# Optimization experiments

Measured on AMD Instinct MI355X. Metric: run time of the kernel, lower is better.

Reference implementation:

```python
import jax, jax.numpy as jnp
import numpy as np
from math import sqrt

RELATIVE_CUTOFF = 128
VALUE_DIM = 64


def _skew(m):
    # m: (b, h, S, 2S-1) -> (b, h, S, S), out[i, j] = m[i, j - i + S - 1]
    b, h, S, _ = m.shape
    m = jnp.pad(m, ((0, 0), (0, 0), (0, 0), (0, 1)))          # (b,h,S,2S)
    m = m.reshape(b, h, 2 * S * S)
    m = jnp.pad(m, ((0, 0), (0, 0), (0, S - 1)))
    m = m.reshape(b, h, S + 1, 2 * S - 1)
    return m[:, :, :S, S - 1:]


def setup_inputs() -> dict:
    key = jax.random.key(0)
    ks = jax.random.split(key, 5)
    B, S, E, H, Dk, Dv = 2, 2048, 512, 8, 64, 64
    return {
        "xs": jax.random.normal(ks[0], (B, S, E), dtype=jnp.float32),
        "w_q": jax.random.normal(ks[1], (H, E, Dk), dtype=jnp.float32) * (1.0 / sqrt(E)),
        "w_k": jax.random.normal(ks[2], (H, E, Dk), dtype=jnp.float32) * (1.0 / sqrt(E)),
        "w_v": jax.random.normal(ks[3], (H, E, Dv), dtype=jnp.float32) * (1.0 / sqrt(E)),
        "w_o": jnp.ones((H,), dtype=jnp.float32),
        "a_k": jax.random.normal(ks[4], (2 * RELATIVE_CUTOFF + 1, Dk), dtype=jnp.float32) * 0.1,
    }


def reference(xs, w_q, w_k, w_v, w_o, a_k):
    S = xs.shape[1]
    queries = jnp.einsum("bse,heq->bhsq", xs, w_q)
    keys = jnp.einsum("bse,hek->bhsk", xs, w_k)
    values = jnp.einsum("bse,hev->bhsv", xs, w_v)

    # relative positional embeddings: pos in [-S+1, S-1], clamped to cutoff
    pos = jnp.clip(jnp.arange(-S + 1, S), -RELATIVE_CUTOFF, RELATIVE_CUTOFF) + RELATIVE_CUTOFF
    rel = a_k[pos]                                             # (2S-1, Dk)

    q_k = jnp.einsum("bhiq,bhjq->bhij", queries, keys)
    q_rel = _skew(jnp.einsum("bhiq,rq->bhir", queries, rel))   # (b,h,S,S)

    e = (q_k + q_rel) / sqrt(VALUE_DIM)
    alphas = jax.nn.softmax(e, axis=3)
    z = jnp.einsum("bhij,bhjv->bhiv", alphas, values)
    return jnp.einsum("bhsv,h->bsv", z, w_o)
```

## Files before the change

kernel.cpp:

```cpp
#include <hip/hip_runtime.h>
#include <hip/hip_bf16.h>

#define S_LEN 2048
#define E_DIM 512
#define D_DIM 64
#define H_NUM 8
#define B_NUM 2
#define BH_NUM 16
#define NQA 257
#define QAE_W 512
#define KSPLIT 2
#define NT (S_LEN / KSPLIT / 64)
#define QTILE 256

typedef _Float16 half8 __attribute__((ext_vector_type(8)));
typedef float f32x16 __attribute__((ext_vector_type(16)));
typedef unsigned int uint2v __attribute__((ext_vector_type(2)));
typedef unsigned int uint4v __attribute__((ext_vector_type(4)));

static __device__ __forceinline__ f32x16 MFMA(half8 a, half8 b, f32x16 c) {
    return __builtin_amdgcn_mfma_f32_32x32x16_f16(a, b, c, 0, 0, 0);
}
static __device__ __forceinline__ f32x16 ZERO16() {
    f32x16 z;
    #pragma unroll
    for (int i = 0; i < 16; ++i) z[i] = 0.f;
    return z;
}
static __device__ __forceinline__ unsigned int PKRTZ(float a, float b) {
    return __builtin_bit_cast(unsigned int, __builtin_amdgcn_cvt_pkrtz(a, b));
}

__global__ __launch_bounds__(256) void cast_x_kernel(
    const float* __restrict__ xs, _Float16* __restrict__ Xh)
{
    const int idx = (blockIdx.x * 256 + threadIdx.x) * 8;
    float4 a = *(const float4*)&xs[idx];
    float4 b = *(const float4*)&xs[idx + 4];
    half8 o;
    o[0] = (_Float16)a.x; o[1] = (_Float16)a.y; o[2] = (_Float16)a.z; o[3] = (_Float16)a.w;
    o[4] = (_Float16)b.x; o[5] = (_Float16)b.y; o[6] = (_Float16)b.z; o[7] = (_Float16)b.w;
    *(half8*)&Xh[idx] = o;
}

__global__ __launch_bounds__(256) void cast_wak_kernel(
    const float* __restrict__ w_q, const float* __restrict__ w_k,
    const float* __restrict__ w_v, const float* __restrict__ w_o,
    const float* __restrict__ a_k,
    _Float16* __restrict__ Wht, _Float16* __restrict__ akh)
{
    __shared__ float T[64][68];
    const int type = blockIdx.z;
    const int t = threadIdx.x;
    if (type == 3) {
        const int bn = blockIdx.y * 8 + blockIdx.x;
        if (bn >= 9) return;
        const int idx = (bn * 256 + t) * 8;
        if (idx < NQA * 64) {
            float4 a = *(const float4*)&a_k[idx];
            float4 b = *(const float4*)&a_k[idx + 4];
            half8 o;
            o[0] = (_Float16)a.x; o[1] = (_Float16)a.y; o[2] = (_Float16)a.z; o[3] = (_Float16)a.w;
            o[4] = (_Float16)b.x; o[5] = (_Float16)b.y; o[6] = (_Float16)b.z; o[7] = (_Float16)b.w;
            *(half8*)&akh[idx] = o;
        }
        return;
    }
    const int kt = blockIdx.x, h = blockIdx.y;
    const float* W = (type == 0) ? w_q : (type == 1) ? w_k : w_v;
    const float scale = (type == 0) ? 0.125f : (type == 2 ? w_o[h] : 1.0f);
    const int kr = t >> 2, nseg = (t & 3) * 16;
    #pragma unroll
    for (int i = 0; i < 4; ++i)
        *(float4*)&T[kr][nseg + 4 * i] =
            *(const float4*)&W[((size_t)h * 512 + kt * 64 + kr) * 64 + nseg + 4 * i];
    __syncthreads();
    const int nr = t >> 2, kseg = (t & 3) * 16;
    _Float16* dst = Wht + ((size_t)(type * 8 + h) * 64 + nr) * 512 + kt * 64 + kseg;
    #pragma unroll
    for (int i = 0; i < 2; ++i) {
        half8 o;
        #pragma unroll
        for (int j = 0; j < 8; ++j) o[j] = (_Float16)(T[kseg + 8 * i + j][nr] * scale);
        *(half8*)&dst[8 * i] = o;
    }
}

__global__ __launch_bounds__(256) void proj_mfma_kernel(
    const _Float16* __restrict__ Xh, const _Float16* __restrict__ Wht,
    const _Float16* __restrict__ akh,
    _Float16* __restrict__ Qh, _Float16* __restrict__ Kh,
    _Float16* __restrict__ Vt, _Float16* __restrict__ QAe)
{
    __shared__ __align__(16) _Float16 raw[30208];
    _Float16 (*Xlds)[128][72] = (_Float16(*)[128][72])raw;
    _Float16 (*Wlds)[64][72]  = (_Float16(*)[64][72])(raw + 18432);
    _Float16* ob  = raw;
    _Float16 (*ak)[72] = (_Float16(*)[72])(raw + 9216);
    _Float16* SLo = raw + 29952;
    _Float16* SHi = raw + 30080;

    const int mt = blockIdx.x, bh = blockIdx.y, type = blockIdx.z;
    const int b = bh >> 3, h = bh & 7;
    const int m0 = mt * 128;
    const int t = threadIdx.x, wid = t >> 6, lane = t & 63;
    const int lq = lane & 31, lh = lane >> 5;

    const _Float16* W = Wht + (size_t)(type * 8 + h) * 64 * 512;
    const _Float16* X = Xh + ((size_t)b * S_LEN + m0) * 512;

    const int xrow = t >> 1, xseg = (t & 1) * 32;
    const int wrow = t >> 2, wseg = (t & 3) * 16;

    #pragma unroll
    for (int i = 0; i < 4; ++i)
        *(half8*)&Xlds[0][xrow][xseg + 8 * i] =
            *(const half8*)&X[(size_t)xrow * 512 + xseg + 8 * i];
    #pragma unroll
    for (int i = 0; i < 2; ++i)
        *(half8*)&Wlds[0][wrow][wseg + 8 * i] =
            *(const half8*)&W[(size_t)wrow * 512 + wseg + 8 * i];
    __syncthreads();

    f32x16 acc[2];
    acc[0] = ZERO16(); acc[1] = ZERO16();
    int cur = 0;
    for (int c = 0; c < 8; ++c) {
        half8 xst[4], wst[2];
        if (c < 7) {
            const int k0 = (c + 1) * 64;
            #pragma unroll
            for (int i = 0; i < 4; ++i)
                xst[i] = *(const half8*)&X[(size_t)xrow * 512 + k0 + xseg + 8 * i];
            #pragma unroll
            for (int i = 0; i < 2; ++i)
                wst[i] = *(const half8*)&W[(size_t)wrow * 512 + k0 + wseg + 8 * i];
        }
        #pragma unroll
        for (int kc = 0; kc < 4; ++kc) {
            half8 a  = *(const half8*)&Xlds[cur][wid * 32 + lq][kc * 16 + lh * 8];
            half8 b0 = *(const half8*)&Wlds[cur][lq][kc * 16 + lh * 8];
            half8 b1 = *(const half8*)&Wlds[cur][32 + lq][kc * 16 + lh * 8];
            acc[0] = MFMA(a, b0, acc[0]);
            acc[1] = MFMA(a, b1, acc[1]);
        }
        if (c < 7) {
            #pragma unroll
            for (int i = 0; i < 4; ++i)
                *(half8*)&Xlds[cur ^ 1][xrow][xseg + 8 * i] = xst[i];
            #pragma unroll
            for (int i = 0; i < 2; ++i)
                *(half8*)&Wlds[cur ^ 1][wrow][wseg + 8 * i] = wst[i];
        }
        __syncthreads();
        cur ^= 1;
    }

    #pragma unroll
    for (int n = 0; n < 2; ++n)
        #pragma unroll
        for (int r = 0; r < 16; ++r) {
            int row = wid * 32 + (r & 3) + ((r >> 2) << 3) + (lh << 2);
            ob[row * 72 + n * 32 + lq] = (_Float16)acc[n][r];
        }
    __syncthreads();

    if (type == 2) {
        const int v = t >> 2, sseg = (t & 3) * 32;
        _Float16* dst = Vt + ((size_t)bh * 64 + v) * S_LEN + m0 + sseg;
        #pragma unroll
        for (int i = 0; i < 4; ++i) {
            half8 o;
            #pragma unroll
            for (int j = 0; j < 8; ++j) o[j] = ob[(sseg + 8 * i + j) * 72 + v];
            *(half8*)&dst[8 * i] = o;
        }
        return;
    }

    {
        _Float16* P = (type == 0) ? Qh : Kh;
        const int row = t >> 1, seg = (t & 1) * 32;
        _Float16* dst = P + ((size_t)bh * S_LEN + m0 + row) * 64 + seg;
        #pragma unroll
        for (int i = 0; i < 4; ++i)
            *(half8*)&dst[8 * i] = *(const half8*)&ob[row * 72 + seg + 8 * i];
    }
    if (type != 0) return;

    for (int r = t; r < 288; r += 256) {
        if (r < NQA) {
            #pragma unroll
            for (int i = 0; i < 8; ++i)
                *(half8*)&ak[r][8 * i] = *(const half8*)&akh[(size_t)r * 64 + 8 * i];
        } else {
            half8 z = {};
            #pragma unroll
            for (int i = 0; i < 8; ++i) *(half8*)&ak[r][8 * i] = z;
        }
    }
    __syncthreads();

    half8 qfr[4];
    #pragma unroll
    for (int kc = 0; kc < 4; ++kc)
        qfr[kc] = *(const half8*)&ob[(wid * 32 + lq) * 72 + kc * 16 + lh * 8];

    for (int nsub = 0; nsub < 9; ++nsub) {
        f32x16 qa = ZERO16();
        #pragma unroll
        for (int kc = 0; kc < 4; ++kc) {
            half8 bf = *(const half8*)&ak[nsub * 32 + lq][kc * 16 + lh * 8];
            qa = MFMA(qfr[kc], bf, qa);
        }
        const int col = nsub * 32 + lq;
        if (col < NQA) {
            #pragma unroll
            for (int r = 0; r < 16; ++r) {
                const int row = m0 + wid * 32 + (r & 3) + ((r >> 2) << 3) + (lh << 2);
                const _Float16 v = (_Float16)qa[r];
                QAe[((size_t)bh * S_LEN + row) * QAE_W + col + 128] = v;
                if (col == 0)   SLo[row - m0] = v;
                if (col == 256) SHi[row - m0] = v;
            }
        }
    }
    __syncthreads();

    const int prow = t >> 1, pseg = (t & 1) * 64;
    const _Float16 lo = SLo[prow], hi = SHi[prow];
    half8 vlo, vhi;
    #pragma unroll
    for (int j = 0; j < 8; ++j) { vlo[j] = lo; vhi[j] = hi; }
    _Float16* pb = QAe + ((size_t)bh * S_LEN + m0 + prow) * QAE_W;
    #pragma unroll
    for (int i = 0; i < 8; ++i) {
        *(half8*)&pb[pseg + 8 * i] = vlo;
        *(half8*)&pb[384 + pseg + 8 * i] = vhi;
    }
}

__global__ __launch_bounds__(512) void attn_kernel(
    const _Float16* __restrict__ Qh, const _Float16* __restrict__ Kh,
    const _Float16* __restrict__ Vt, const _Float16* __restrict__ QAe,
    _Float16* __restrict__ Po, float2* __restrict__ Ml)
{
    __shared__ __align__(16) char smraw[36864];
    _Float16 (*Klds)[64][72] = (_Float16(*)[64][72])smraw;
    _Float16 (*Vlds)[64][72] = (_Float16(*)[64][72])(smraw + 18432);
    _Float16* Obuf = (_Float16*)smraw;
    __shared__ __align__(16) _Float16 Bnd[8][32][128];

    const int p0 = blockIdx.x;
    const int nb = (p0 & 7) * 32 + (p0 >> 3);
    const int bh = nb >> 4;
    const int rem = nb & 15;
    const int qt = rem & 7, ks = rem >> 3;
    const int i0 = qt * QTILE;

    const int t = threadIdx.x, wid = t >> 6, lane = t & 63;
    const int lq = lane & 31, lh = lane >> 5;
    const int i0w = i0 + wid * 32;
    const int qg = i0w + lq;

    half8 qf[4];
    #pragma unroll
    for (int kc = 0; kc < 4; ++kc)
        qf[kc] = *(const half8*)&Qh[((size_t)bh * S_LEN + qg) * 64 + kc * 16 + lh * 8];

    const _Float16* qaeRow = QAe + ((size_t)bh * S_LEN + qg) * QAE_W;
    const float qa_lo = (float)qaeRow[128];
    const float qa_hi = (float)qaeRow[384];
    const _Float16* BndSrc = QAe + ((size_t)bh * S_LEN + i0w) * QAE_W;

    float rm = -1e30f, rl = 0.f;
    f32x16 acco[2];
    acco[0] = ZERO16(); acco[1] = ZERO16();

    const int srow = t >> 3, sseg = (t & 7) * 8;
    const _Float16* Kbase = Kh + (size_t)bh * S_LEN * 64;
    const _Float16* Vbase = Vt + ((size_t)bh * 64 + srow) * S_LEN;

    const int brow = lane >> 4;
    const int bcol = (lane & 15) * 8;

    half8 kst, vst, breg[8];
    const int kv0 = ks * 64;
    *(half8*)&Klds[0][srow][sseg] = *(const half8*)&Kbase[(size_t)(kv0 + srow) * 64 + sseg];
    *(half8*)&Vlds[0][srow][sseg] = *(const half8*)&Vbase[kv0 + sseg];
    kst = *(const half8*)&Kbase[(size_t)(kv0 + 128 + srow) * 64 + sseg];
    vst = *(const half8*)&Vbase[kv0 + 128 + sseg];

    bool inb_next;
    {
        const int d0 = kv0 - i0w;
        inb_next = (d0 < 159) && (d0 > -191);
        if (inb_next) {
            const int cw0n = (d0 + 225) & ~7;
            #pragma unroll
            for (int ps = 0; ps < 8; ++ps)
                breg[ps] = *(const half8*)&BndSrc[(size_t)(ps * 4 + brow) * QAE_W + cw0n + bcol];
        }
    }
    __syncthreads();

    for (int jt = 0; jt < NT; ++jt) {
        const int cur = jt & 1;
        if (jt) __syncthreads();
        if (jt + 1 < NT) {
            *(half8*)&Klds[cur ^ 1][srow][sseg] = kst;
            *(half8*)&Vlds[cur ^ 1][srow][sseg] = vst;
        }
        if (jt + 2 < NT) {
            const int jg = kv0 + (jt + 2) * 128;
            kst = *(const half8*)&Kbase[(size_t)(jg + srow) * 64 + sseg];
            vst = *(const half8*)&Vbase[jg + sseg];
        }

        const int diff = kv0 + jt * 128 - i0w;
        const bool inband = inb_next;
        const int cw0 = (diff + 225) & ~7;

        if (inband) {
            #pragma unroll
            for (int ps = 0; ps < 8; ++ps)
                *(half8*)&Bnd[wid][ps * 4 + brow][bcol] = breg[ps];
        }
        {
            const int dn = diff + 128;
            inb_next = (jt + 1 < NT) && (dn < 159) && (dn > -191);
            if (inb_next) {
                const int cw0n = (dn + 225) & ~7;
                #pragma unroll
                for (int ps = 0; ps < 8; ++ps)
                    breg[ps] = *(const half8*)&BndSrc[(size_t)(ps * 4 + brow) * QAE_W + cw0n + bcol];
            }
        }

        f32x16 accs[2];
        accs[0] = ZERO16(); accs[1] = ZERO16();
        __builtin_amdgcn_s_setprio(1);
        #pragma unroll
        for (int kc = 0; kc < 4; ++kc) {
            half8 ka = *(const half8*)&Klds[cur][lq][kc * 16 + lh * 8];
            half8 kb = *(const half8*)&Klds[cur][32 + lq][kc * 16 + lh * 8];
            accs[0] = MFMA(ka, qf[kc], accs[0]);
            accs[1] = MFMA(kb, qf[kc], accs[1]);
        }
        __builtin_amdgcn_s_setprio(0);

        const bool allhi = (diff >= 159);
        const bool alllo = (diff <= -191);
        float bunif = 0.f;
        if (allhi) bunif = qa_hi;
        else if (alllo) bunif = qa_lo;
        else {
            asm volatile("s_waitcnt lgkmcnt(0)" ::: "memory");
            __builtin_amdgcn_sched_barrier(0);
            const int pb = diff + 256 - cw0 - lq;
            #pragma unroll
            for (int m = 0; m < 2; ++m)
                #pragma unroll
                for (int r = 0; r < 16; ++r) {
                    const int keyoff = m * 32 + (r & 3) + ((r >> 2) << 3) + (lh << 2);
                    accs[m][r] += (float)Bnd[wid][lq][pb + keyoff];
                }
        }

        float t8[8];
        #pragma unroll
        for (int i = 0; i < 8; ++i)
            t8[i] = fmaxf(fmaxf(accs[0][i], accs[0][i + 8]),
                          fmaxf(accs[1][i], accs[1][i + 8]));
        float tmax = fmaxf(fmaxf(fmaxf(t8[0], t8[1]), fmaxf(t8[2], t8[3])),
                           fmaxf(fmaxf(t8[4], t8[5]), fmaxf(t8[6], t8[7])));
        tmax = fmaxf(tmax, __shfl_xor(tmax, 32));
        const float mnew = fmaxf(rm, tmax + bunif);
        const bool resc = __any(mnew > rm);
        const float corr = __expf(rm - mnew);
        const float shift = mnew - bunif;
        rm = mnew;

        #pragma unroll
        for (int m = 0; m < 2; ++m)
            #pragma unroll
            for (int r = 0; r < 16; ++r)
                accs[m][r] = __expf(accs[m][r] - shift);

        float s8[8];
        #pragma unroll
        for (int i = 0; i < 8; ++i)
            s8[i] = (accs[0][i] + accs[0][i + 8]) + (accs[1][i] + accs[1][i + 8]);
        float psum = ((s8[0] + s8[1]) + (s8[2] + s8[3])) +
                     ((s8[4] + s8[5]) + (s8[6] + s8[7]));
        psum += __shfl_xor(psum, 32);

        if (resc) {
            rl = rl * corr + psum;
            #pragma unroll
            for (int n = 0; n < 2; ++n)
                #pragma unroll
                for (int r = 0; r < 16; ++r) acco[n][r] *= corr;
        } else {
            rl += psum;
        }

        half8 pf[4];
        #pragma unroll
        for (int kc = 0; kc < 4; ++kc) {
            const int m = kc >> 1, rb = (kc & 1) * 8;
            unsigned int a01 = PKRTZ(accs[m][rb + 0], accs[m][rb + 1]);
            unsigned int a45 = PKRTZ(accs[m][rb + 4], accs[m][rb + 5]);
            unsigned int a23 = PKRTZ(accs[m][rb + 2], accs[m][rb + 3]);
            unsigned int a67 = PKRTZ(accs[m][rb + 6], accs[m][rb + 7]);
            uint2v r02 = __builtin_amdgcn_permlane32_swap(a01, a45, false, false);
            uint2v r13 = __builtin_amdgcn_permlane32_swap(a23, a67, false, false);
            uint4v wv;
            wv[0] = r02[0]; wv[1] = r13[0]; wv[2] = r02[1]; wv[3] = r13[1];
            pf[kc] = __builtin_bit_cast(half8, wv);
        }

        __builtin_amdgcn_s_setprio(1);
        #pragma unroll
        for (int kc = 0; kc < 4; ++kc) {
            half8 v0 = *(const half8*)&Vlds[cur][lq][kc * 16 + lh * 8];
            half8 v1 = *(const half8*)&Vlds[cur][32 + lq][kc * 16 + lh * 8];
            acco[0] = MFMA(v0, pf[kc], acco[0]);
            acco[1] = MFMA(v1, pf[kc], acco[1]);
        }
        __builtin_amdgcn_s_setprio(0);
    }

    __syncthreads();
    const int orow = wid * 32 + lq;
    #pragma unroll
    for (int n = 0; n < 2; ++n)
        #pragma unroll
        for (int rq = 0; rq < 4; ++rq) {
            uint2v hv;
            hv[0] = PKRTZ(acco[n][rq * 4 + 0], acco[n][rq * 4 + 1]);
            hv[1] = PKRTZ(acco[n][rq * 4 + 2], acco[n][rq * 4 + 3]);
            *(uint2v*)&Obuf[(size_t)orow * 72 + n * 32 + rq * 8 + lh * 4] = hv;
        }
    if (lh == 0)
        Ml[((size_t)ks * BH_NUM + bh) * S_LEN + qg] = make_float2(rm, rl);
    asm volatile("s_waitcnt lgkmcnt(0)" ::: "memory");
    __builtin_amdgcn_sched_barrier(0);
    const int rrow = wid * 32 + (lane >> 1);
    const int rseg = (lane & 1) * 32;
    _Float16* dst = Po + (((size_t)ks * BH_NUM + bh) * S_LEN + i0 + rrow) * 64 + rseg;
    #pragma unroll
    for (int i = 0; i < 4; ++i)
        *(half8*)&dst[8 * i] = *(const half8*)&Obuf[(size_t)rrow * 72 + rseg + 8 * i];
}

__global__ __launch_bounds__(256) void merge_kernel(
    const _Float16* __restrict__ Po, const float2* __restrict__ Ml,
    float* __restrict__ out)
{
    const int b = blockIdx.y;
    const int s = blockIdx.x * 32 + (threadIdx.x >> 3);
    const int v0 = (threadIdx.x & 7) * 8;
    float acc[8] = {0, 0, 0, 0, 0, 0, 0, 0};
    #pragma unroll
    for (int h = 0; h < 8; ++h) {
        const int bh = b * 8 + h;
        float m[KSPLIT], l[KSPLIT];
        #pragma unroll
        for (int p = 0; p < KSPLIT; ++p) {
            const float2 v = Ml[((size_t)p * BH_NUM + bh) * S_LEN + s];
            m[p] = v.x; l[p] = v.y;
        }
        float M = fmaxf(m[0], m[1]);
        float L = 0.f, w[KSPLIT];
        #pragma unroll
        for (int p = 0; p < KSPLIT; ++p) { w[p] = __expf(m[p] - M); L += w[p] * l[p]; }
        const float invL = 1.0f / L;
        #pragma unroll
        for (int p = 0; p < KSPLIT; ++p) {
            half8 o = *(const half8*)&Po[(((size_t)p * BH_NUM + bh) * S_LEN + s) * 64 + v0];
            const float wp = w[p] * invL;
            #pragma unroll
            for (int j = 0; j < 8; ++j) acc[j] += wp * (float)o[j];
        }
    }
    float4 o0 = {acc[0], acc[1], acc[2], acc[3]};
    float4 o1 = {acc[4], acc[5], acc[6], acc[7]};
    *(float4*)&out[((size_t)b * S_LEN + s) * 64 + v0] = o0;
    *(float4*)&out[((size_t)b * S_LEN + s) * 64 + v0 + 4] = o1;
}

extern "C" void kernel_launch(void* const* d_in, const int* in_sizes, int n_in,
                              void* d_out, int out_size, void* d_ws, size_t ws_size,
                              hipStream_t stream)
{
    const float* xs  = (const float*)d_in[0];
    const float* w_q = (const float*)d_in[1];
    const float* w_k = (const float*)d_in[2];
    const float* w_v = (const float*)d_in[3];
    const float* w_o = (const float*)d_in[4];
    const float* a_k = (const float*)d_in[5];
    float* out = (float*)d_out;

    char* w = (char*)d_ws;
    _Float16* Xh  = (_Float16*)w;  w += (size_t)B_NUM * S_LEN * E_DIM * 2;
    _Float16* Wht = (_Float16*)w;  w += (size_t)3 * H_NUM * 64 * 512 * 2;
    _Float16* akh = (_Float16*)w;  w += 33024;
    _Float16* Qh  = (_Float16*)w;  w += (size_t)BH_NUM * S_LEN * 64 * 2;
    _Float16* Kh  = (_Float16*)w;  w += (size_t)BH_NUM * S_LEN * 64 * 2;
    _Float16* Vt  = (_Float16*)w;  w += (size_t)BH_NUM * S_LEN * 64 * 2;
    _Float16* QAe = (_Float16*)w;  w += (size_t)BH_NUM * S_LEN * QAE_W * 2;
    _Float16* Po  = (_Float16*)w;  w += (size_t)KSPLIT * BH_NUM * S_LEN * 64 * 2;
    float2*   Ml  = (float2*)w;

    cast_x_kernel<<<1024, 256, 0, stream>>>(xs, Xh);
    cast_wak_kernel<<<dim3(8, 8, 4), 256, 0, stream>>>(w_q, w_k, w_v, w_o, a_k, Wht, akh);
    proj_mfma_kernel<<<dim3(16, 16, 3), 256, 0, stream>>>(Xh, Wht, akh, Qh, Kh, Vt, QAe);
    attn_kernel<<<256, 512, 0, stream>>>(Qh, Kh, Vt, QAe, Po, Ml);
    merge_kernel<<<dim3(64, 2), 256, 0, stream>>>(Po, Ml, out);
}
```

Measured before the change: 80.06 us.

## Process two 64-key tiles per iteration with wider relative-bias band buffer

Restructures the attention loop so each iteration handles 128 keys (two 64-row K/V tiles) instead of 64, halving the number of online-softmax max/rescale steps and loop iterations. The relative-position band buffer is widened to 176 columns and loaded with a new per-row lane mapping so one load covers both tiles. K/V staging now uses two sync barriers per iteration with register prefetch of the next pair. This raises register pressure (four score accumulators, more staging registers) and LDS use, which may lower occupancy, and pads the QAe workspace to keep the wider band reads in bounds.

```diff
diff --git a/kernel.cpp b/kernel.cpp
--- a/kernel.cpp
+++ b/kernel.cpp
@@ -10,8 +10,9 @@
 #define NQA 257
 #define QAE_W 512
 #define KSPLIT 2
-#define NT (S_LEN / KSPLIT / 64)
+#define NP 8
 #define QTILE 256
+#define BNDW 176
 
 typedef _Float16 half8 __attribute__((ext_vector_type(8)));
 typedef float f32x16 __attribute__((ext_vector_type(16)));
@@ -249,7 +250,7 @@
     _Float16 (*Klds)[64][72] = (_Float16(*)[64][72])smraw;
     _Float16 (*Vlds)[64][72] = (_Float16(*)[64][72])(smraw + 18432);
     _Float16* Obuf = (_Float16*)smraw;
-    __shared__ __align__(16) _Float16 Bnd[8][32][128];
+    __shared__ __align__(16) _Float16 Bnd[8][32][BNDW];
 
     const int p0 = blockIdx.x;
     const int nb = (p0 & 7) * 32 + (p0 >> 3);
@@ -257,6 +258,7 @@
     const int rem = nb & 15;
     const int qt = rem & 7, ks = rem >> 3;
     const int i0 = qt * QTILE;
+    const int kv0 = ks * 128;
 
     const int t = threadIdx.x, wid = t >> 6, lane = t & 63;
     const int lq = lane & 31, lh = lane >> 5;
@@ -281,90 +283,103 @@
     const _Float16* Kbase = Kh + (size_t)bh * S_LEN * 64;
     const _Float16* Vbase = Vt + ((size_t)bh * 64 + srow) * S_LEN;
 
-    const int brow = lane >> 4;
-    const int bcol = (lane & 15) * 8;
-
-    half8 kst, vst, breg[8];
-    const int kv0 = ks * 64;
-    *(half8*)&Klds[0][srow][sseg] = *(const half8*)&Kbase[(size_t)(kv0 + srow) * 64 + sseg];
-    *(half8*)&Vlds[0][srow][sseg] = *(const half8*)&Vbase[kv0 + sseg];
-    kst = *(const half8*)&Kbase[(size_t)(kv0 + 128 + srow) * 64 + sseg];
-    vst = *(const half8*)&Vbase[kv0 + 128 + sseg];
-
-    bool inb_next;
+    const int brow = lane >> 1;
+    const int bhalf = (lane & 1) * 88;
+
+    half8 kA, kB, vA, vB, breg[11];
     {
-        const int d0 = kv0 - i0w;
-        inb_next = (d0 < 159) && (d0 > -191);
-        if (inb_next) {
-            const int cw0n = (d0 + 225) & ~7;
-            #pragma unroll
-            for (int ps = 0; ps < 8; ++ps)
-                breg[ps] = *(const half8*)&BndSrc[(size_t)(ps * 4 + brow) * QAE_W + cw0n + bcol];
-        }
-    }
-    __syncthreads();
-
-    for (int jt = 0; jt < NT; ++jt) {
-        const int cur = jt & 1;
-        if (jt) __syncthreads();
-        if (jt + 1 < NT) {
-            *(half8*)&Klds[cur ^ 1][srow][sseg] = kst;
-            *(half8*)&Vlds[cur ^ 1][srow][sseg] = vst;
-        }
-        if (jt + 2 < NT) {
-            const int jg = kv0 + (jt + 2) * 128;
-            kst = *(const half8*)&Kbase[(size_t)(jg + srow) * 64 + sseg];
-            vst = *(const half8*)&Vbase[jg + sseg];
-        }
-
-        const int diff = kv0 + jt * 128 - i0w;
-        const bool inband = inb_next;
-        const int cw0 = (diff + 225) & ~7;
-
-        if (inband) {
-            #pragma unroll
-            for (int ps = 0; ps < 8; ++ps)
-                *(half8*)&Bnd[wid][ps * 4 + brow][bcol] = breg[ps];
-        }
-        {
-            const int dn = diff + 128;
-            inb_next = (jt + 1 < NT) && (dn < 159) && (dn > -191);
-            if (inb_next) {
-                const int cw0n = (dn + 225) & ~7;
-                #pragma unroll
-                for (int ps = 0; ps < 8; ++ps)
-                    breg[ps] = *(const half8*)&BndSrc[(size_t)(ps * 4 + brow) * QAE_W + cw0n + bcol];
-            }
-        }
-
-        f32x16 accs[2];
-        accs[0] = ZERO16(); accs[1] = ZERO16();
+        const int js = kv0;
+        *(half8*)&Klds[0][srow][sseg] = *(const half8*)&Kbase[(size_t)(js + srow) * 64 + sseg];
+        *(half8*)&Klds[1][srow][sseg] = *(const half8*)&Kbase[(size_t)(js + 64 + srow) * 64 + sseg];
+        *(half8*)&Vlds[0][srow][sseg] = *(const half8*)&Vbase[js + sseg];
+        *(half8*)&Vlds[1][srow][sseg] = *(const half8*)&Vbase[js + 64 + sseg];
+        const int j1 = 256 + kv0;
+        kA = *(const half8*)&Kbase[(size_t)(j1 + srow) * 64 + sseg];
+        kB = *(const half8*)&Kbase[(size_t)(j1 + 64 + srow) * 64 + sseg];
+        vA = *(const half8*)&Vbase[j1 + sseg];
+        vB = *(const half8*)&Vbase[j1 + 64 + sseg];
+    }
+    bool bA_n, bB_n; int cw0_n = 0;
+    {
+        const int d = kv0 - i0w;
+        bA_n = (d > -191) && (d < 159);
+        bB_n = (d > -255) && (d < 95);
+        if (bA_n || bB_n) {
+            const int dFB = bA_n ? d : d + 64;
+            cw0_n = (dFB + 225) & ~7;
+            cw0_n = cw0_n > 336 ? 336 : cw0_n;
+            #pragma unroll
+            for (int i = 0; i < 11; ++i)
+                breg[i] = *(const half8*)&BndSrc[(size_t)brow * QAE_W + cw0_n + bhalf + i * 8];
+        }
+    }
+    __syncthreads();
+
+    for (int p = 0; p < NP; ++p) {
+        const int diff = p * 256 + kv0 - i0w;
+        const bool bA = bA_n, bB = bB_n;
+        const int cw0 = cw0_n;
+
+        if (bA || bB) {
+            #pragma unroll
+            for (int i = 0; i < 11; ++i)
+                *(half8*)&Bnd[wid][brow][bhalf + i * 8] = breg[i];
+        }
+
+        f32x16 accs[4];
+        accs[0] = ZERO16(); accs[1] = ZERO16(); accs[2] = ZERO16(); accs[3] = ZERO16();
         __builtin_amdgcn_s_setprio(1);
         #pragma unroll
         for (int kc = 0; kc < 4; ++kc) {
-            half8 ka = *(const half8*)&Klds[cur][lq][kc * 16 + lh * 8];
-            half8 kb = *(const half8*)&Klds[cur][32 + lq][kc * 16 + lh * 8];
-            accs[0] = MFMA(ka, qf[kc], accs[0]);
-            accs[1] = MFMA(kb, qf[kc], accs[1]);
+            half8 a0 = *(const half8*)&Klds[0][lq][kc * 16 + lh * 8];
+            half8 a1 = *(const half8*)&Klds[0][32 + lq][kc * 16 + lh * 8];
+            half8 b0 = *(const half8*)&Klds[1][lq][kc * 16 + lh * 8];
+            half8 b1 = *(const half8*)&Klds[1][32 + lq][kc * 16 + lh * 8];
+            accs[0] = MFMA(a0, qf[kc], accs[0]);
+            accs[1] = MFMA(a1, qf[kc], accs[1]);
+            accs[2] = MFMA(b0, qf[kc], accs[2]);
+            accs[3] = MFMA(b1, qf[kc], accs[3]);
         }
         __builtin_amdgcn_s_setprio(0);
 
-        const bool allhi = (diff >= 159);
-        const bool alllo = (diff <= -191);
         float bunif = 0.f;
-        if (allhi) bunif = qa_hi;
-        else if (alllo) bunif = qa_lo;
-        else {
+        if (diff >= 159) {
+            bunif = qa_hi;
+        } else if (diff <= -255) {
+            bunif = qa_lo;
+        } else {
             asm volatile("s_waitcnt lgkmcnt(0)" ::: "memory");
             __builtin_amdgcn_sched_barrier(0);
-            const int pb = diff + 256 - cw0 - lq;
-            #pragma unroll
-            for (int m = 0; m < 2; ++m)
+            const int pbA = diff + 256 - cw0 - lq;
+            const int pbB = pbA + 64;
+            if (bA) {
                 #pragma unroll
-                for (int r = 0; r < 16; ++r) {
-                    const int keyoff = m * 32 + (r & 3) + ((r >> 2) << 3) + (lh << 2);
-                    accs[m][r] += (float)Bnd[wid][lq][pb + keyoff];
-                }
+                for (int m = 0; m < 2; ++m)
+                    #pragma unroll
+                    for (int r = 0; r < 16; ++r) {
+                        const int keyoff = m * 32 + (r & 3) + ((r >> 2) << 3) + (lh << 2);
+                        accs[m][r] += (float)Bnd[wid][lq][pbA + keyoff];
+                    }
+            } else {
+                #pragma unroll
+                for (int m = 0; m < 2; ++m)
+                    #pragma unroll
+                    for (int r = 0; r < 16; ++r) accs[m][r] += qa_lo;
+            }
+            if (bB) {
+                #pragma unroll
+                for (int m = 0; m < 2; ++m)
+                    #pragma unroll
+                    for (int r = 0; r < 16; ++r) {
+                        const int keyoff = m * 32 + (r & 3) + ((r >> 2) << 3) + (lh << 2);
+                        accs[2 + m][r] += (float)Bnd[wid][lq][pbB + keyoff];
+                    }
+            } else {
+                #pragma unroll
+                for (int m = 0; m < 2; ++m)
+                    #pragma unroll
+                    for (int r = 0; r < 16; ++r) accs[2 + m][r] += qa_hi;
+            }
         }
 
         float t8[8];
@@ -372,6 +387,10 @@
         for (int i = 0; i < 8; ++i)
             t8[i] = fmaxf(fmaxf(accs[0][i], accs[0][i + 8]),
                           fmaxf(accs[1][i], accs[1][i + 8]));
+        #pragma unroll
+        for (int i = 0; i < 8; ++i)
+            t8[i] = fmaxf(t8[i], fmaxf(fmaxf(accs[2][i], accs[2][i + 8]),
+                                       fmaxf(accs[3][i], accs[3][i + 8])));
         float tmax = fmaxf(fmaxf(fmaxf(t8[0], t8[1]), fmaxf(t8[2], t8[3])),
                            fmaxf(fmaxf(t8[4], t8[5]), fmaxf(t8[6], t8[7])));
         tmax = fmaxf(tmax, __shfl_xor(tmax, 32));
@@ -382,15 +401,16 @@
         rm = mnew;
 
         #pragma unroll
-        for (int m = 0; m < 2; ++m)
+        for (int s = 0; s < 4; ++s)
             #pragma unroll
             for (int r = 0; r < 16; ++r)
-                accs[m][r] = __expf(accs[m][r] - shift);
+                accs[s][r] = __expf(accs[s][r] - shift);
 
         float s8[8];
         #pragma unroll
         for (int i = 0; i < 8; ++i)
-            s8[i] = (accs[0][i] + accs[0][i + 8]) + (accs[1][i] + accs[1][i + 8]);
+            s8[i] = ((accs[0][i] + accs[0][i + 8]) + (accs[1][i] + accs[1][i + 8]))
+                  + ((accs[2][i] + accs[2][i + 8]) + (accs[3][i] + accs[3][i + 8]));
         float psum = ((s8[0] + s8[1]) + (s8[2] + s8[3])) +
                      ((s8[4] + s8[5]) + (s8[6] + s8[7]));
         psum += __shfl_xor(psum, 32);
@@ -405,30 +425,81 @@
             rl += psum;
         }
 
-        half8 pf[4];
+        half8 pfA[4], pfB[4];
         #pragma unroll
         for (int kc = 0; kc < 4; ++kc) {
-            const int m = kc >> 1, rb = (kc & 1) * 8;
-            unsigned int a01 = PKRTZ(accs[m][rb + 0], accs[m][rb + 1]);
-            unsigned int a45 = PKRTZ(accs[m][rb + 4], accs[m][rb + 5]);
-            unsigned int a23 = PKRTZ(accs[m][rb + 2], accs[m][rb + 3]);
-            unsigned int a67 = PKRTZ(accs[m][rb + 6], accs[m][rb + 7]);
-            uint2v r02 = __builtin_amdgcn_permlane32_swap(a01, a45, false, false);
-            uint2v r13 = __builtin_amdgcn_permlane32_swap(a23, a67, false, false);
-            uint4v wv;
-            wv[0] = r02[0]; wv[1] = r13[0]; wv[2] = r02[1]; wv[3] = r13[1];
-            pf[kc] = __builtin_bit_cast(half8, wv);
+            {
+                const int m = kc >> 1, rb = (kc & 1) * 8;
+                unsigned int a01 = PKRTZ(accs[m][rb + 0], accs[m][rb + 1]);
+                unsigned int a45 = PKRTZ(accs[m][rb + 4], accs[m][rb + 5]);
+                unsigned int a23 = PKRTZ(accs[m][rb + 2], accs[m][rb + 3]);
+                unsigned int a67 = PKRTZ(accs[m][rb + 6], accs[m][rb + 7]);
+                uint2v r02 = __builtin_amdgcn_permlane32_swap(a01, a45, false, false);
+                uint2v r13 = __builtin_amdgcn_permlane32_swap(a23, a67, false, false);
+                uint4v wv;
+                wv[0] = r02[0]; wv[1] = r13[0]; wv[2] = r02[1]; wv[3] = r13[1];
+                pfA[kc] = __builtin_bit_cast(half8, wv);
+            }
+            {
+                const int m = 2 + (kc >> 1), rb = (kc & 1) * 8;
+                unsigned int a01 = PKRTZ(accs[m][rb + 0], accs[m][rb + 1]);
+                unsigned int a45 = PKRTZ(accs[m][rb + 4], accs[m][rb + 5]);
+                unsigned int a23 = PKRTZ(accs[m][rb + 2], accs[m][rb + 3]);
+                unsigned int a67 = PKRTZ(accs[m][rb + 6], accs[m][rb + 7]);
+                uint2v r02 = __builtin_amdgcn_permlane32_swap(a01, a45, false, false);
+                uint2v r13 = __builtin_amdgcn_permlane32_swap(a23, a67, false, false);
+                uint4v wv;
+                wv[0] = r02[0]; wv[1] = r13[0]; wv[2] = r02[1]; wv[3] = r13[1];
+                pfB[kc] = __builtin_bit_cast(half8, wv);
+            }
         }
 
         __builtin_amdgcn_s_setprio(1);
         #pragma unroll
         for (int kc = 0; kc < 4; ++kc) {
-            half8 v0 = *(const half8*)&Vlds[cur][lq][kc * 16 + lh * 8];
-            half8 v1 = *(const half8*)&Vlds[cur][32 + lq][kc * 16 + lh * 8];
-            acco[0] = MFMA(v0, pf[kc], acco[0]);
-            acco[1] = MFMA(v1, pf[kc], acco[1]);
+            half8 v0 = *(const half8*)&Vlds[0][lq][kc * 16 + lh * 8];
+            half8 v1 = *(const half8*)&Vlds[0][32 + lq][kc * 16 + lh * 8];
+            acco[0] = MFMA(v0, pfA[kc], acco[0]);
+            acco[1] = MFMA(v1, pfA[kc], acco[1]);
+        }
+        #pragma unroll
+        for (int kc = 0; kc < 4; ++kc) {
+            half8 v0 = *(const half8*)&Vlds[1][lq][kc * 16 + lh * 8];
+            half8 v1 = *(const half8*)&Vlds[1][32 + lq][kc * 16 + lh * 8];
+            acco[0] = MFMA(v0, pfB[kc], acco[0]);
+            acco[1] = MFMA(v1, pfB[kc], acco[1]);
         }
         __builtin_amdgcn_s_setprio(0);
+
+        {
+            const int dn = diff + 256;
+            bA_n = (p + 1 < NP) && (dn > -191) && (dn < 159);
+            bB_n = (p + 1 < NP) && (dn > -255) && (dn < 95);
+            if (bA_n || bB_n) {
+                const int dFB = bA_n ? dn : dn + 64;
+                cw0_n = (dFB + 225) & ~7;
+                cw0_n = cw0_n > 336 ? 336 : cw0_n;
+                #pragma unroll
+                for (int i = 0; i < 11; ++i)
+                    breg[i] = *(const half8*)&BndSrc[(size_t)brow * QAE_W + cw0_n + bhalf + i * 8];
+            }
+        }
+
+        if (p + 1 < NP) {
+            __syncthreads();
+            *(half8*)&Klds[0][srow][sseg] = kA;
+            *(half8*)&Klds[1][srow][sseg] = kB;
+            *(half8*)&Vlds[0][srow][sseg] = vA;
+            *(half8*)&Vlds[1][srow][sseg] = vB;
+            if (p + 2 < NP) {
+                const int jn = (p + 2) * 256 + kv0;
+                kA = *(const half8*)&Kbase[(size_t)(jn + srow) * 64 + sseg];
+                kB = *(const half8*)&Kbase[(size_t)(jn + 64 + srow) * 64 + sseg];
+                vA = *(const half8*)&Vbase[jn + sseg];
+                vB = *(const half8*)&Vbase[jn + 64 + sseg];
+            }
+            __syncthreads();
+        }
     }
 
     __syncthreads();
@@ -509,7 +580,7 @@
     _Float16* Qh  = (_Float16*)w;  w += (size_t)BH_NUM * S_LEN * 64 * 2;
     _Float16* Kh  = (_Float16*)w;  w += (size_t)BH_NUM * S_LEN * 64 * 2;
     _Float16* Vt  = (_Float16*)w;  w += (size_t)BH_NUM * S_LEN * 64 * 2;
-    _Float16* QAe = (_Float16*)w;  w += (size_t)BH_NUM * S_LEN * QAE_W * 2;
+    _Float16* QAe = (_Float16*)w;  w += (size_t)BH_NUM * S_LEN * QAE_W * 2 + 1024;
     _Float16* Po  = (_Float16*)w;  w += (size_t)KSPLIT * BH_NUM * S_LEN * 64 * 2;
     float2*   Ml  = (float2*)w;
 
```

Result: no change. 79.69 us, median of 2 (-0.5%).

## Split attention keys four ways with interleaved 64-key tiles and shared band buffer

Applied to the files above, without the earlier changes.

Raises the key split from 2 to 4, doubling the attention grid to 512 blocks, with each block handling interleaved 64-key tiles strided by 256. It drops the double-buffered K/V shared memory in favour of a single buffer plus register prefetch, and replaces the per-wave band buffer with a block-wide 256x72 relative-bias tile loaded cooperatively. Per-lane band handling now selects between uniform and banded bias. The aim is more parallelism and occupancy through smaller shared memory and a launch-bounds hint. The cost is an extra sync per tile, less load/compute overlap, and more partial results for the merge kernel to combine.

```diff
diff --git a/kernel.cpp b/kernel.cpp
--- a/kernel.cpp
+++ b/kernel.cpp
@@ -9,9 +9,10 @@
 #define BH_NUM 16
 #define NQA 257
 #define QAE_W 512
-#define KSPLIT 2
-#define NT (S_LEN / KSPLIT / 64)
+#define KSPLIT 4
+#define NTL 8
 #define QTILE 256
+#define BNDW 72
 
 typedef _Float16 half8 __attribute__((ext_vector_type(8)));
 typedef float f32x16 __attribute__((ext_vector_type(16)));
@@ -240,23 +241,23 @@
     }
 }
 
-__global__ __launch_bounds__(512) void attn_kernel(
+__global__ __launch_bounds__(512, 4) void attn_kernel(
     const _Float16* __restrict__ Qh, const _Float16* __restrict__ Kh,
     const _Float16* __restrict__ Vt, const _Float16* __restrict__ QAe,
     _Float16* __restrict__ Po, float2* __restrict__ Ml)
 {
-    __shared__ __align__(16) char smraw[36864];
-    _Float16 (*Klds)[64][72] = (_Float16(*)[64][72])smraw;
-    _Float16 (*Vlds)[64][72] = (_Float16(*)[64][72])(smraw + 18432);
-    _Float16* Obuf = (_Float16*)smraw;
-    __shared__ __align__(16) _Float16 Bnd[8][32][128];
+    __shared__ __align__(16) _Float16 Klds[64][72];
+    __shared__ __align__(16) _Float16 Vlds[64][72];
+    __shared__ __align__(16) _Float16 Bnd[QTILE][BNDW];
+    _Float16* Obuf = &Bnd[0][0];
 
     const int p0 = blockIdx.x;
-    const int nb = (p0 & 7) * 32 + (p0 >> 3);
-    const int bh = nb >> 4;
-    const int rem = nb & 15;
+    const int nb = (p0 & 7) * 64 + (p0 >> 3);
+    const int bh = nb >> 5;
+    const int rem = nb & 31;
     const int qt = rem & 7, ks = rem >> 3;
     const int i0 = qt * QTILE;
+    const int kv0 = ks * 64;
 
     const int t = threadIdx.x, wid = t >> 6, lane = t & 63;
     const int lq = lane & 31, lh = lane >> 5;
@@ -271,7 +272,7 @@
     const _Float16* qaeRow = QAe + ((size_t)bh * S_LEN + qg) * QAE_W;
     const float qa_lo = (float)qaeRow[128];
     const float qa_hi = (float)qaeRow[384];
-    const _Float16* BndSrc = QAe + ((size_t)bh * S_LEN + i0w) * QAE_W;
+    const _Float16* QAeB = QAe + (size_t)bh * S_LEN * QAE_W;
 
     float rm = -1e30f, rl = 0.f;
     f32x16 acco[2];
@@ -281,89 +282,85 @@
     const _Float16* Kbase = Kh + (size_t)bh * S_LEN * 64;
     const _Float16* Vbase = Vt + ((size_t)bh * 64 + srow) * S_LEN;
 
-    const int brow = lane >> 4;
-    const int bcol = (lane & 15) * 8;
-
-    half8 kst, vst, breg[8];
-    const int kv0 = ks * 64;
-    *(half8*)&Klds[0][srow][sseg] = *(const half8*)&Kbase[(size_t)(kv0 + srow) * 64 + sseg];
-    *(half8*)&Vlds[0][srow][sseg] = *(const half8*)&Vbase[kv0 + sseg];
-    kst = *(const half8*)&Kbase[(size_t)(kv0 + 128 + srow) * 64 + sseg];
-    vst = *(const half8*)&Vbase[kv0 + 128 + sseg];
-
-    bool inb_next;
-    {
-        const int d0 = kv0 - i0w;
-        inb_next = (d0 < 159) && (d0 > -191);
-        if (inb_next) {
-            const int cw0n = (d0 + 225) & ~7;
-            #pragma unroll
-            for (int ps = 0; ps < 8; ++ps)
-                breg[ps] = *(const half8*)&BndSrc[(size_t)(ps * 4 + brow) * QAE_W + cw0n + bcol];
-        }
-    }
-    __syncthreads();
-
-    for (int jt = 0; jt < NT; ++jt) {
-        const int cur = jt & 1;
+    const int browS = t >> 1, bselS = t & 1;
+
+    half8 kA, vA;
+    kA = *(const half8*)&Kbase[(size_t)(kv0 + srow) * 64 + sseg];
+    vA = *(const half8*)&Vbase[kv0 + sseg];
+
+    for (int jt = 0; jt < NTL; ++jt) {
+        const int J = jt * 256 + kv0;
+        const int X0 = J - i0 + 256;
+
         if (jt) __syncthreads();
-        if (jt + 1 < NT) {
-            *(half8*)&Klds[cur ^ 1][srow][sseg] = kst;
-            *(half8*)&Vlds[cur ^ 1][srow][sseg] = vst;
-        }
-        if (jt + 2 < NT) {
-            const int jg = kv0 + (jt + 2) * 128;
-            kst = *(const half8*)&Kbase[(size_t)(jg + srow) * 64 + sseg];
-            vst = *(const half8*)&Vbase[jg + sseg];
-        }
-
-        const int diff = kv0 + jt * 128 - i0w;
-        const bool inband = inb_next;
-        const int cw0 = (diff + 225) & ~7;
-
-        if (inband) {
-            #pragma unroll
-            for (int ps = 0; ps < 8; ++ps)
-                *(half8*)&Bnd[wid][ps * 4 + brow][bcol] = breg[ps];
-        }
-        {
-            const int dn = diff + 128;
-            inb_next = (jt + 1 < NT) && (dn < 159) && (dn > -191);
-            if (inb_next) {
-                const int cw0n = (dn + 225) & ~7;
-                #pragma unroll
-                for (int ps = 0; ps < 8; ++ps)
-                    breg[ps] = *(const half8*)&BndSrc[(size_t)(ps * 4 + brow) * QAE_W + cw0n + bcol];
+        *(half8*)&Klds[srow][sseg] = kA;
+        *(half8*)&Vlds[srow][sseg] = vA;
+
+        if (X0 >= 66 && X0 <= 638) {
+            int a = (X0 - browS) & ~7;
+            a = min(max(a, 0), QAE_W - BNDW);
+            const _Float16* src = QAeB + (size_t)(i0 + browS) * QAE_W + a;
+            if (bselS == 0) {
+                half8 b0 = *(const half8*)&src[0];
+                half8 b1 = *(const half8*)&src[8];
+                half8 b2 = *(const half8*)&src[16];
+                half8 b3 = *(const half8*)&src[24];
+                half8 b4 = *(const half8*)&src[32];
+                *(half8*)&Bnd[browS][0]  = b0;
+                *(half8*)&Bnd[browS][8]  = b1;
+                *(half8*)&Bnd[browS][16] = b2;
+                *(half8*)&Bnd[browS][24] = b3;
+                *(half8*)&Bnd[browS][32] = b4;
+            } else {
+                half8 b0 = *(const half8*)&src[40];
+                half8 b1 = *(const half8*)&src[48];
+                half8 b2 = *(const half8*)&src[56];
+                half8 b3 = *(const half8*)&src[64];
+                *(half8*)&Bnd[browS][40] = b0;
+                *(half8*)&Bnd[browS][48] = b1;
+                *(half8*)&Bnd[browS][56] = b2;
+                *(half8*)&Bnd[browS][64] = b3;
             }
         }
+        if (jt + 1 < NTL) {
+            const int Jn = (jt + 1) * 256 + kv0;
+            kA = *(const half8*)&Kbase[(size_t)(Jn + srow) * 64 + sseg];
+            vA = *(const half8*)&Vbase[Jn + sseg];
+        }
+        __syncthreads();
 
         f32x16 accs[2];
         accs[0] = ZERO16(); accs[1] = ZERO16();
         __builtin_amdgcn_s_setprio(1);
         #pragma unroll
         for (int kc = 0; kc < 4; ++kc) {
-            half8 ka = *(const half8*)&Klds[cur][lq][kc * 16 + lh * 8];
-            half8 kb = *(const half8*)&Klds[cur][32 + lq][kc * 16 + lh * 8];
+            half8 ka = *(const half8*)&Klds[lq][kc * 16 + lh * 8];
+            half8 kb = *(const half8*)&Klds[32 + lq][kc * 16 + lh * 8];
             accs[0] = MFMA(ka, qf[kc], accs[0]);
             accs[1] = MFMA(kb, qf[kc], accs[1]);
         }
         __builtin_amdgcn_s_setprio(0);
 
-        const bool allhi = (diff >= 159);
-        const bool alllo = (diff <= -191);
+        const int xw = X0 - wid * 32;
         float bunif = 0.f;
-        if (allhi) bunif = qa_hi;
-        else if (alllo) bunif = qa_lo;
-        else {
-            asm volatile("s_waitcnt lgkmcnt(0)" ::: "memory");
-            __builtin_amdgcn_sched_barrier(0);
-            const int pb = diff + 256 - cw0 - lq;
+        if (xw - 31 >= 384) {
+            bunif = qa_hi;
+        } else if (xw <= 65) {
+            bunif = qa_lo;
+        } else {
+            const int xl = xw - lq;
+            const bool lhi = xl >= 384, llo = xl <= 65;
+            const float lu = lhi ? qa_hi : qa_lo;
+            const bool lband = !(lhi || llo);
+            const int rowL = wid * 32 + lq;
+            const int base = xl & 7;
             #pragma unroll
             for (int m = 0; m < 2; ++m)
                 #pragma unroll
                 for (int r = 0; r < 16; ++r) {
                     const int keyoff = m * 32 + (r & 3) + ((r >> 2) << 3) + (lh << 2);
-                    accs[m][r] += (float)Bnd[wid][lq][pb + keyoff];
+                    const float bv = (float)Bnd[rowL][base + keyoff];
+                    accs[m][r] += lband ? bv : lu;
                 }
         }
 
@@ -423,8 +420,8 @@
         __builtin_amdgcn_s_setprio(1);
         #pragma unroll
         for (int kc = 0; kc < 4; ++kc) {
-            half8 v0 = *(const half8*)&Vlds[cur][lq][kc * 16 + lh * 8];
-            half8 v1 = *(const half8*)&Vlds[cur][32 + lq][kc * 16 + lh * 8];
+            half8 v0 = *(const half8*)&Vlds[lq][kc * 16 + lh * 8];
+            half8 v1 = *(const half8*)&Vlds[32 + lq][kc * 16 + lh * 8];
             acco[0] = MFMA(v0, pf[kc], acco[0]);
             acco[1] = MFMA(v1, pf[kc], acco[1]);
         }
@@ -471,7 +468,7 @@
             const float2 v = Ml[((size_t)p * BH_NUM + bh) * S_LEN + s];
             m[p] = v.x; l[p] = v.y;
         }
-        float M = fmaxf(m[0], m[1]);
+        float M = fmaxf(fmaxf(m[0], m[1]), fmaxf(m[2], m[3]));
         float L = 0.f, w[KSPLIT];
         #pragma unroll
         for (int p = 0; p < KSPLIT; ++p) { w[p] = __expf(m[p] - M); L += w[p] * l[p]; }
@@ -509,13 +506,13 @@
     _Float16* Qh  = (_Float16*)w;  w += (size_t)BH_NUM * S_LEN * 64 * 2;
     _Float16* Kh  = (_Float16*)w;  w += (size_t)BH_NUM * S_LEN * 64 * 2;
     _Float16* Vt  = (_Float16*)w;  w += (size_t)BH_NUM * S_LEN * 64 * 2;
-    _Float16* QAe = (_Float16*)w;  w += (size_t)BH_NUM * S_LEN * QAE_W * 2;
+    _Float16* QAe = (_Float16*)w;  w += (size_t)BH_NUM * S_LEN * QAE_W * 2 + 1024;
     _Float16* Po  = (_Float16*)w;  w += (size_t)KSPLIT * BH_NUM * S_LEN * 64 * 2;
     float2*   Ml  = (float2*)w;
 
     cast_x_kernel<<<1024, 256, 0, stream>>>(xs, Xh);
     cast_wak_kernel<<<dim3(8, 8, 4), 256, 0, stream>>>(w_q, w_k, w_v, w_o, a_k, Wht, akh);
     proj_mfma_kernel<<<dim3(16, 16, 3), 256, 0, stream>>>(Xh, Wht, akh, Qh, Kh, Vt, QAe);
-    attn_kernel<<<256, 512, 0, stream>>>(Qh, Kh, Vt, QAe, Po, Ml);
+    attn_kernel<<<512, 512, 0, stream>>>(Qh, Kh, Vt, QAe, Po, Ml);
     merge_kernel<<<dim3(64, 2), 256, 0, stream>>>(Po, Ml, out);
 }
```

New measurement: 84.46 us. 5.5% more time.
